# Kernel optimization log

Hardware: AMD Instinct MI355X
Metric: run time of the kernel (lower is better)

Reference implementation:

```python
import jax, jax.numpy as jnp
import numpy as np

EPS = 1e-6

def _rmsnorm(x, w):
    var = jnp.mean(x * x, axis=-1, keepdims=True)
    return w * (x * jax.lax.rsqrt(var + EPS))

def _rope(t, cos, sin):
    # t: [B,S,H,d_k]; cos/sin: [S,d_k/2] -> complex multiply on (even,odd) pairs
    B, S, H, D = t.shape
    tr = t.reshape(B, S, H, D // 2, 2)
    t0, t1 = tr[..., 0], tr[..., 1]
    c = cos[None, :, None, :]
    s = sin[None, :, None, :]
    o0 = t0 * c - t1 * s
    o1 = t0 * s + t1 * c
    return jnp.stack([o0, o1], axis=-1).reshape(B, S, H, D)

def setup_inputs() -> dict:
    key = jax.random.key(0)
    ks = jax.random.split(key, 9)
    B, S, D, H, DFF = 1, 4096, 1024, 16, 4096
    dk = D // H
    hidden = int(2 * DFF / 3)  # 2730, SwiGLU hidden dim
    sc = 0.02
    x = jax.random.normal(ks[0], (B, S, D), jnp.float32)
    # RoPE tables (theta=10000)
    inv_freq = 1.0 / (10000.0 ** (np.arange(0, dk, 2, dtype=np.float32) / dk))
    ang = np.outer(np.arange(S, dtype=np.float32), inv_freq)
    freqs_cos = jnp.asarray(np.cos(ang))
    freqs_sin = jnp.asarray(np.sin(ang))
    # causal additive mask [1,1,S,S]
    mask = jnp.where(np.tril(np.ones((S, S), bool)), 0.0, -1e9).astype(jnp.float32)[None, None]
    Wq = jax.random.normal(ks[1], (D, D), jnp.float32) * sc
    Wk = jax.random.normal(ks[2], (D, D), jnp.float32) * sc
    Wv = jax.random.normal(ks[3], (D, D), jnp.float32) * sc
    Wo = jax.random.normal(ks[4], (D, D), jnp.float32) * sc
    ln1_w = jnp.ones((D,), jnp.float32)
    ln2_w = jnp.ones((D,), jnp.float32)
    w1 = jax.random.normal(ks[5], (D, hidden), jnp.float32) * sc
    w2 = jax.random.normal(ks[6], (hidden, D), jnp.float32) * sc
    w3 = jax.random.normal(ks[7], (D, hidden), jnp.float32) * sc
    return dict(x=x, freqs_cos=freqs_cos, freqs_sin=freqs_sin, mask=mask,
                Wq=Wq, Wk=Wk, Wv=Wv, Wo=Wo, ln1_w=ln1_w, ln2_w=ln2_w,
                w1=w1, w2=w2, w3=w3)

def reference(x, freqs_cos, freqs_sin, mask, Wq, Wk, Wv, Wo, ln1_w, ln2_w, w1, w2, w3):
    B, S, D = x.shape
    H = 16
    dk = D // H
    scale = jnp.sqrt(jnp.float32(dk))
    # attention sublayer (pre-RMSNorm)
    h = _rmsnorm(x, ln1_w)
    Q = (h @ Wq).reshape(B, S, H, dk)
    K = (h @ Wk).reshape(B, S, H, dk)
    V = (h @ Wv).reshape(B, S, H, dk)
    Q = _rope(Q, freqs_cos, freqs_sin)
    K = _rope(K, freqs_cos, freqs_sin)
    scores = jnp.einsum('bshd,bthd->bhst', Q, K) / scale + mask  # [B,H,S,S]
    attn = jax.nn.softmax(scores, axis=-1)
    ctx = jnp.einsum('bhst,bthd->bshd', attn, V).reshape(B, S, D)
    x = x + ctx @ Wo
    # SwiGLU FFN sublayer
    h2 = _rmsnorm(x, ln2_w)
    ff = (jax.nn.silu(h2 @ w1) * (h2 @ w3)) @ w2
    x = x + ff
    return x
```

## Files before the change

### kernel.cpp

```cpp
#include <hip/hip_runtime.h>

#define S_LEN 4096
#define D_MODEL 1024
#define NHEAD 16
#define DK 64
#define HID 2730
#define HIDP 2880
#define QKV_LD 3072

typedef unsigned short u16;
typedef unsigned int u32;
typedef __bf16 bf16x8 __attribute__((ext_vector_type(8)));
typedef float f32x4 __attribute__((ext_vector_type(4)));

#define MFMA16 __builtin_amdgcn_mfma_f32_16x16x32_bf16
#define EXP2 __builtin_amdgcn_exp2f

__device__ __forceinline__ float b2f(u16 u) {
    return __builtin_bit_cast(float, (u32)u << 16);
}
__device__ __forceinline__ u16 f2b(float f) {
    u32 u = __builtin_bit_cast(u32, f);
    u += 0x7FFF + ((u >> 16) & 1);
    return (u16)(u >> 16);
}
__device__ __forceinline__ u32 pk_trunc(float lo, float hi) {
    return __builtin_amdgcn_perm(__builtin_bit_cast(u32, hi),
                                 __builtin_bit_cast(u32, lo), 0x07060302u);
}
__device__ __forceinline__ void gll16(const u16* g, u16* l) {
    __builtin_amdgcn_global_load_lds(
        (__attribute__((address_space(1))) void*)(g),
        (__attribute__((address_space(3))) void*)(l),
        16, 0, 0);
}

__global__ __launch_bounds__(256)
void prep_k(const float* s0, const float* s1, const float* s2,
            const float* s3, const float* s4, const float* s5,
            const float* s6, u16* d0, u16* d1, u16* d2, u16* d3,
            u16* d4, u16* d5, u16* d6,
            const float* __restrict__ x, const float* __restrict__ ln1,
            u16* __restrict__ hb) {
    __shared__ float t[32][33];
    __shared__ float red[4];
    const int bid = blockIdx.x;
    const int tid = threadIdx.x;

    if (bid >= 12736) {
        const int row = bid - 12736;
        const float4 v = ((const float4*)(x + (size_t)row * D_MODEL))[tid];
        float ss = v.x * v.x + v.y * v.y + v.z * v.z + v.w * v.w;
        for (int o = 32; o; o >>= 1) ss += __shfl_down(ss, o);
        if ((tid & 63) == 0) red[tid >> 6] = ss;
        __syncthreads();
        const float tot = red[0] + red[1] + red[2] + red[3];
        const float rs = rsqrtf(tot * (1.0f / D_MODEL) + 1e-6f);
        const float4 wv = ((const float4*)ln1)[tid];
        u16* op = hb + (size_t)row * D_MODEL + tid * 4;
        u32 p0 = (u32)f2b(v.x * rs * wv.x) | ((u32)f2b(v.y * rs * wv.y) << 16);
        u32 p1 = (u32)f2b(v.z * rs * wv.z) | ((u32)f2b(v.w * rs * wv.w) << 16);
        uint2 pk; pk.x = p0; pk.y = p1;
        *(uint2*)op = pk;
        return;
    }

    const float* srcs[7] = {s0, s1, s2, s3, s4, s5, s6};
    u16* dsts[7] = {d0, d1, d2, d3, d4, d5, d6};
    const int RR[7] = {1024, 1024, 1024, 1024, 1024, 1024, 2730};
    const int CC[7] = {1024, 1024, 1024, 1024, 2730, 2730, 1024};
    const int OC[7] = {1024, 1024, 1024, 1024, 1024, 1024, 2880};
    const int XD[7] = {32, 32, 32, 32, 32, 32, 90};

    int seg, start;
    if (bid < 4096)      { seg = bid >> 10; start = seg << 10; }
    else if (bid < 6976) { seg = 4; start = 4096; }
    else if (bid < 9856) { seg = 5; start = 6976; }
    else                 { seg = 6; start = 9856; }
    const int local = bid - start;
    const int bx = local % XD[seg], byy = local / XD[seg];
    const float* in = srcs[seg];
    u16* out = dsts[seg];
    const int R = RR[seg], C = CC[seg], outC = OC[seg];

    const int r0 = byy * 32;
    const int c0 = bx * 32;
    const int tx = tid & 31, ty = tid >> 5;
#pragma unroll
    for (int j = 0; j < 4; ++j) {
        int ir = c0 + ty + j * 8;
        int ic = r0 + tx;
        t[ty + j * 8][tx] = (ir < R && ic < C) ? in[(size_t)ir * C + ic] : 0.0f;
    }
    __syncthreads();
#pragma unroll
    for (int j = 0; j < 4; ++j)
        out[(size_t)(r0 + ty + j * 8) * outC + c0 + tx] = f2b(t[tx][ty + j * 8]);
}

__global__ __launch_bounds__(256)
void rmsnorm_k(const float* __restrict__ x, const float* __restrict__ w,
               u16* __restrict__ out) {
    const int row = blockIdx.x;
    const int tid = threadIdx.x;
    const float4 v = ((const float4*)(x + (size_t)row * D_MODEL))[tid];
    float ss = v.x * v.x + v.y * v.y + v.z * v.z + v.w * v.w;
    for (int o = 32; o; o >>= 1) ss += __shfl_down(ss, o);
    __shared__ float red[4];
    if ((tid & 63) == 0) red[tid >> 6] = ss;
    __syncthreads();
    const float tot = red[0] + red[1] + red[2] + red[3];
    const float rs = rsqrtf(tot * (1.0f / D_MODEL) + 1e-6f);
    const float4 wv = ((const float4*)w)[tid];
    u16* op = out + (size_t)row * D_MODEL + tid * 4;
    u32 p0 = (u32)f2b(v.x * rs * wv.x) | ((u32)f2b(v.y * rs * wv.y) << 16);
    u32 p1 = (u32)f2b(v.z * rs * wv.z) | ((u32)f2b(v.w * rs * wv.w) << 16);
    uint2 pk; pk.x = p0; pk.y = p1;
    *(uint2*)op = pk;
}

__global__ __launch_bounds__(256)
void packkv_k(const u16* __restrict__ qkv, const float* __restrict__ fc,
              const float* __restrict__ fs, u16* __restrict__ vt,
              u16* __restrict__ kp) {
    __shared__ u16 t[32][33];
    const int h = blockIdx.z;
    const int t0 = blockIdx.x * 32;
    const int d0 = blockIdx.y * 32;
    const int tx = threadIdx.x, ty = threadIdx.y;
#pragma unroll
    for (int j = 0; j < 4; ++j)
        t[ty + j * 8][tx] =
            qkv[(size_t)(t0 + ty + j * 8) * QKV_LD + 2 * D_MODEL + h * DK + d0 + tx];

    const int id = ty * 32 + tx;
    const int sA = t0 + (id >> 3);
    const int dA = d0 + (id & 7) * 4;
    uint2 kvp = *(const uint2*)(qkv + (size_t)sA * QKV_LD + D_MODEL + h * DK + dA);
    const int fi = sA * 32 + (dA >> 1);
    const float cc0 = fc[fi], ss0 = fs[fi];
    const float cc1 = fc[fi + 1], ss1 = fs[fi + 1];
    auto rpk = [](u32 w, float c, float s) -> u32 {
        const float a = b2f((u16)w), b = b2f((u16)(w >> 16));
        return (u32)f2b(a * c - b * s) | ((u32)f2b(a * s + b * c) << 16);
    };
    kvp.x = rpk(kvp.x, cc0, ss0);
    kvp.y = rpk(kvp.y, cc1, ss1);
    *(uint2*)(kp + ((size_t)h * S_LEN + sA) * DK + dA) = kvp;

    __syncthreads();
#pragma unroll
    for (int j = 0; j < 4; ++j)
        vt[(size_t)h * DK * S_LEN + (size_t)(d0 + ty + j * 8) * S_LEN + t0 + tx] =
            t[tx][ty + j * 8];
}

template <int EPI>
__global__ __launch_bounds__(256)
void gemm128(const u16* __restrict__ A, int lda, const u16* __restrict__ Bt, int ldb,
             void* __restrict__ C, int ldc, int K, const float* __restrict__ resid) {
    const int m0 = blockIdx.y * 128, n0 = blockIdx.x * 128;
    const int tid = threadIdx.x;
    const int wave = tid >> 6, lane = tid & 63;
    const int wr = wave >> 1, wc = wave & 1;
    const int r16 = lane & 15, kq = lane >> 4;

    __shared__ __align__(16) u16 As[128 * 32];
    __shared__ __align__(16) u16 Bs[128 * 32];

    const int srow = tid >> 2, sk = (tid & 3) * 8;
    const u16* ag0 = A + (size_t)(m0 + srow) * lda + sk;
    const u16* ag1 = A + (size_t)(m0 + 64 + srow) * lda + sk;
    const u16* bg0 = Bt + (size_t)(n0 + srow) * ldb + sk;
    const u16* bg1 = Bt + (size_t)(n0 + 64 + srow) * ldb + sk;
    u16* asw = As + wave * 512;
    u16* bsw = Bs + wave * 512;

    f32x4 acc[16];
#pragma unroll
    for (int i = 0; i < 16; ++i) acc[i] = f32x4{0.f, 0.f, 0.f, 0.f};

    for (int k0 = 0; k0 < K; k0 += 32) {
        __syncthreads();
        gll16(ag0 + k0, asw);
        gll16(ag1 + k0, asw + 2048);
        gll16(bg0 + k0, bsw);
        gll16(bg1 + k0, bsw + 2048);
        __syncthreads();
        bf16x8 af[4], bf[4];
#pragma unroll
        for (int mt = 0; mt < 4; ++mt)
            af[mt] = *(const bf16x8*)&As[(wr * 64 + mt * 16 + r16) * 32 + kq * 8];
#pragma unroll
        for (int nt = 0; nt < 4; ++nt)
            bf[nt] = *(const bf16x8*)&Bs[(wc * 64 + nt * 16 + r16) * 32 + kq * 8];
#pragma unroll
        for (int mt = 0; mt < 4; ++mt)
#pragma unroll
            for (int nt = 0; nt < 4; ++nt)
                acc[mt * 4 + nt] = MFMA16(af[mt], bf[nt], acc[mt * 4 + nt], 0, 0, 0);
    }

#pragma unroll
    for (int mt = 0; mt < 4; ++mt) {
#pragma unroll
        for (int nt = 0; nt < 4; ++nt) {
            const int col = n0 + wc * 64 + nt * 16 + r16;
#pragma unroll
            for (int j = 0; j < 4; ++j) {
                const int row = m0 + wr * 64 + mt * 16 + kq * 4 + j;
                if (EPI == 0) {
                    ((u16*)C)[(size_t)row * ldc + col] = f2b(acc[mt * 4 + nt][j]);
                } else {
                    ((float*)C)[(size_t)row * ldc + col] =
                        resid[(size_t)row * ldc + col] + acc[mt * 4 + nt][j];
                }
            }
        }
    }
}

__global__ __launch_bounds__(256)
void gemm64r(const u16* __restrict__ A, int lda, const u16* __restrict__ Bt, int ldb,
             float* __restrict__ C, int ldc, int K, const float* __restrict__ resid) {
    const int m0 = blockIdx.y * 128, n0 = blockIdx.x * 64;
    const int tid = threadIdx.x;
    const int wave = tid >> 6, lane = tid & 63;
    const int r16 = lane & 15, kq = lane >> 4;

    __shared__ __align__(16) u16 As[128 * 32];
    __shared__ __align__(16) u16 Bs[64 * 32];

    const int srow = tid >> 2, sk = (tid & 3) * 8;
    const u16* ag0 = A + (size_t)(m0 + srow) * lda + sk;
    const u16* ag1 = A + (size_t)(m0 + 64 + srow) * lda + sk;
    const u16* bg = Bt + (size_t)(n0 + srow) * ldb + sk;
    u16* asw = As + wave * 512;
    u16* bsw = Bs + wave * 512;

    f32x4 acc[8];
#pragma unroll
    for (int i = 0; i < 8; ++i) acc[i] = f32x4{0.f, 0.f, 0.f, 0.f};

    for (int k0 = 0; k0 < K; k0 += 32) {
        __syncthreads();
        gll16(ag0 + k0, asw);
        gll16(ag1 + k0, asw + 2048);
        gll16(bg + k0, bsw);
        __syncthreads();
        bf16x8 af[2], bf[4];
#pragma unroll
        for (int mt = 0; mt < 2; ++mt)
            af[mt] = *(const bf16x8*)&As[(wave * 32 + mt * 16 + r16) * 32 + kq * 8];
#pragma unroll
        for (int nt = 0; nt < 4; ++nt)
            bf[nt] = *(const bf16x8*)&Bs[(nt * 16 + r16) * 32 + kq * 8];
#pragma unroll
        for (int mt = 0; mt < 2; ++mt)
#pragma unroll
            for (int nt = 0; nt < 4; ++nt)
                acc[mt * 4 + nt] = MFMA16(af[mt], bf[nt], acc[mt * 4 + nt], 0, 0, 0);
    }

#pragma unroll
    for (int mt = 0; mt < 2; ++mt)
#pragma unroll
        for (int nt = 0; nt < 4; ++nt) {
            const int col = n0 + nt * 16 + r16;
#pragma unroll
            for (int j = 0; j < 4; ++j) {
                const int row = m0 + wave * 32 + mt * 16 + kq * 4 + j;
                C[(size_t)row * ldc + col] =
                    resid[(size_t)row * ldc + col] + acc[mt * 4 + nt][j];
            }
        }
}

__global__ __launch_bounds__(256, 3)
void gemm_dual96(const u16* __restrict__ A, int lda,
                 const u16* __restrict__ B1, const u16* __restrict__ B3, int ldb,
                 u16* __restrict__ C, int ldc, int K) {
    const int m0 = blockIdx.y * 128, n0 = blockIdx.x * 96;
    const int tid = threadIdx.x;
    const int wave = tid >> 6, lane = tid & 63;
    const int wr = wave >> 1, wc = wave & 1;
    const int r16 = lane & 15, kq = lane >> 4;

    __shared__ __align__(16) u16 As[128 * 32];
    __shared__ __align__(16) u16 Bs[192 * 32];

    const int srow = tid >> 2, sk = (tid & 3) * 8;
    const u16* ag0 = A + (size_t)(m0 + srow) * lda + sk;
    const u16* ag1 = A + (size_t)(m0 + 64 + srow) * lda + sk;
    const u16* bp0 = B1 + (size_t)(n0 + srow) * ldb + sk;
    const u16* bp1 = (srow < 32)
        ? B1 + (size_t)(n0 + 64 + srow) * ldb + sk
        : B3 + (size_t)(n0 + srow - 32) * ldb + sk;
    const u16* bp2 = B3 + (size_t)(n0 + 32 + srow) * ldb + sk;
    u16* asw0 = As + wave * 512;
    u16* asw1 = As + 2048 + wave * 512;
    u16* bsw0 = Bs + wave * 512;
    u16* bsw1 = Bs + 2048 + wave * 512;
    u16* bsw2 = Bs + 4096 + wave * 512;

    f32x4 acc1[12], acc3[12];
#pragma unroll
    for (int i = 0; i < 12; ++i) {
        acc1[i] = f32x4{0.f, 0.f, 0.f, 0.f};
        acc3[i] = f32x4{0.f, 0.f, 0.f, 0.f};
    }

    for (int k0 = 0; k0 < K; k0 += 32) {
        __syncthreads();
        gll16(ag0 + k0, asw0);
        gll16(ag1 + k0, asw1);
        gll16(bp0 + k0, bsw0);
        gll16(bp1 + k0, bsw1);
        gll16(bp2 + k0, bsw2);
        __syncthreads();
        bf16x8 af[4], b1f[3], b3f[3];
#pragma unroll
        for (int mt = 0; mt < 4; ++mt)
            af[mt] = *(const bf16x8*)&As[(wr * 64 + mt * 16 + r16) * 32 + kq * 8];
#pragma unroll
        for (int nt = 0; nt < 3; ++nt) {
            b1f[nt] = *(const bf16x8*)&Bs[(wc * 48 + nt * 16 + r16) * 32 + kq * 8];
            b3f[nt] = *(const bf16x8*)&Bs[(96 + wc * 48 + nt * 16 + r16) * 32 + kq * 8];
        }
#pragma unroll
        for (int mt = 0; mt < 4; ++mt)
#pragma unroll
            for (int nt = 0; nt < 3; ++nt) {
                acc1[mt * 3 + nt] = MFMA16(af[mt], b1f[nt], acc1[mt * 3 + nt], 0, 0, 0);
                acc3[mt * 3 + nt] = MFMA16(af[mt], b3f[nt], acc3[mt * 3 + nt], 0, 0, 0);
            }
    }

#pragma unroll
    for (int mt = 0; mt < 4; ++mt)
#pragma unroll
        for (int nt = 0; nt < 3; ++nt) {
            const int col = n0 + wc * 48 + nt * 16 + r16;
#pragma unroll
            for (int j = 0; j < 4; ++j) {
                const int row = m0 + wr * 64 + mt * 16 + kq * 4 + j;
                const float v1 = acc1[mt * 3 + nt][j];
                const float v3 = acc3[mt * 3 + nt][j];
                const float sig = 1.0f / (1.0f + __expf(-v1));
                C[(size_t)row * ldc + col] = f2b(v1 * sig * v3);
            }
        }
}

__global__ __launch_bounds__(256)
void flash_k(const u16* __restrict__ qkv, const u16* __restrict__ vt,
             const u16* __restrict__ kp, const float* __restrict__ fc,
             const float* __restrict__ fs, u16* __restrict__ ctx) {
    const int h = blockIdx.x;
    const int by = blockIdx.y;
    const int hi = by >> 4, lo = by & 15;
    const int base = lo + ((hi >> 1) << 4);
    const int qi = (hi & 1) ? (63 - base) : base;
    const int q0 = qi * 64;
    const int tid = threadIdx.x;
    const int wave = tid >> 6, lane = tid & 63;
    const int r16 = lane & 15, kq = lane >> 4;

    __shared__ __align__(16) u16 Kb[2][64 * 64];
    __shared__ __align__(16) u16 Vb[2][64 * 64];
    __shared__ __align__(16) u16 Ps[4 * 16 * 64];

    const u16* kb = kp + (size_t)h * S_LEN * DK;
    const u16* vb = vt + (size_t)h * DK * S_LEN;
    const int srow = tid >> 3;
    const int lcol = ((tid & 7) ^ (srow & 7)) * 8;
    const int qloc = wave * 16 + r16;
    const int qglob = q0 + qloc;
    const int sw = r16 & 7;
    const int c0 = (kq ^ sw) * 8;
    const int c1 = ((4 ^ kq) ^ sw) * 8;
    const int psw = r16 & 14;
    u16* psrow = Ps + wave * 1024 + r16 * 64;

    const float SC = 0.125f * 1.44269504f;
    const u16* qrow = qkv + (size_t)qglob * QKV_LD + h * DK;
    uint4 uq0 = *(const uint4*)(qrow + kq * 8);
    uint4 uq1 = *(const uint4*)(qrow + 32 + kq * 8);
    const float4 c0v = *(const float4*)(fc + qglob * 32 + kq * 4);
    const float4 s0v = *(const float4*)(fs + qglob * 32 + kq * 4);
    const float4 c1v = *(const float4*)(fc + qglob * 32 + 16 + kq * 4);
    const float4 s1v = *(const float4*)(fs + qglob * 32 + 16 + kq * 4);
    auto rp = [SC](u32 w, float c, float s) -> u32 {
        const float a = b2f((u16)w), b = b2f((u16)(w >> 16));
        return (u32)f2b((a * c - b * s) * SC) |
               ((u32)f2b((a * s + b * c) * SC) << 16);
    };
    uq0.x = rp(uq0.x, c0v.x, s0v.x); uq0.y = rp(uq0.y, c0v.y, s0v.y);
    uq0.z = rp(uq0.z, c0v.z, s0v.z); uq0.w = rp(uq0.w, c0v.w, s0v.w);
    uq1.x = rp(uq1.x, c1v.x, s1v.x); uq1.y = rp(uq1.y, c1v.y, s1v.y);
    uq1.z = rp(uq1.z, c1v.z, s1v.z); uq1.w = rp(uq1.w, c1v.w, s1v.w);
    const bf16x8 qf0 = __builtin_bit_cast(bf16x8, uq0);
    const bf16x8 qf1 = __builtin_bit_cast(bf16x8, uq1);

    f32x4 o[4];
#pragma unroll
    for (int i = 0; i < 4; ++i) o[i] = f32x4{0.f, 0.f, 0.f, 0.f};
    f32x4 lacc = f32x4{0.f, 0.f, 0.f, 0.f};
    const uint4 uone = make_uint4(0x3F803F80u, 0x3F803F80u, 0x3F803F80u, 0x3F803F80u);
    const bf16x8 ones = __builtin_bit_cast(bf16x8, uone);

#pragma unroll
    for (int i = 0; i < 2; ++i) {
        const int r = srow + i * 32;
        gll16(kb + (size_t)r * DK + lcol, Kb[0] + tid * 8 + i * 2048);
        gll16(vb + (size_t)r * S_LEN + lcol, Vb[0] + tid * 8 + i * 2048);
    }

    for (int t = 0; t <= qi; ++t) {
        __syncthreads();
        if (t < qi) {
            const int t1 = (t + 1) * 64;
            u16* kd = Kb[(t + 1) & 1];
            u16* vd = Vb[(t + 1) & 1];
#pragma unroll
            for (int i = 0; i < 2; ++i) {
                const int r = srow + i * 32;
                gll16(kb + (size_t)(t1 + r) * DK + lcol, kd + tid * 8 + i * 2048);
                gll16(vb + (size_t)r * S_LEN + t1 + lcol, vd + tid * 8 + i * 2048);
            }
        }
        const u16* Ks = Kb[t & 1];
        const u16* Vs = Vb[t & 1];

        f32x4 s[4];
#pragma unroll
        for (int nt = 0; nt < 4; ++nt) {
            s[nt] = f32x4{0.f, 0.f, 0.f, 0.f};
            const bf16x8 k0 = *(const bf16x8*)&Ks[(nt * 16 + r16) * 64 + c0];
            s[nt] = MFMA16(k0, qf0, s[nt], 0, 0, 0);
            const bf16x8 k1 = *(const bf16x8*)&Ks[(nt * 16 + r16) * 64 + c1];
            s[nt] = MFMA16(k1, qf1, s[nt], 0, 0, 0);
        }

        float pr[16];
#pragma unroll
        for (int nt = 0; nt < 4; ++nt)
#pragma unroll
            for (int j = 0; j < 4; ++j) pr[nt * 4 + j] = EXP2(s[nt][j]);
        if (t == qi) {
#pragma unroll
            for (int nt = 0; nt < 4; ++nt)
#pragma unroll
                for (int j = 0; j < 4; ++j)
                    if ((nt * 16 + kq * 4 + j) > qloc) pr[nt * 4 + j] = 0.f;
        }

#pragma unroll
        for (int nt = 0; nt < 4; ++nt) {
            uint2 pk;
            pk.x = pk_trunc(pr[nt * 4 + 0], pr[nt * 4 + 1]);
            pk.y = pk_trunc(pr[nt * 4 + 2], pr[nt * 4 + 3]);
            *(uint2*)&psrow[((nt * 4 + kq) ^ psw) * 4] = pk;
        }

#pragma unroll
        for (int ks = 0; ks < 2; ++ks) {
            const bf16x8 pf = *(const bf16x8*)&psrow[((8 * ks + 2 * kq) ^ psw) * 4];
            lacc = MFMA16(ones, pf, lacc, 0, 0, 0);
            const int cv = (((ks << 2) ^ kq) ^ sw) * 8;
#pragma unroll
            for (int nt = 0; nt < 4; ++nt) {
                const bf16x8 vf = *(const bf16x8*)&Vs[(nt * 16 + r16) * 64 + cv];
                o[nt] = MFMA16(vf, pf, o[nt], 0, 0, 0);
            }
        }
    }

    const float inv = 1.0f / lacc[0];
    const size_t row = qglob;
#pragma unroll
    for (int nt = 0; nt < 4; ++nt) {
        uint2 pk;
        pk.x = (u32)f2b(o[nt][0] * inv) | ((u32)f2b(o[nt][1] * inv) << 16);
        pk.y = (u32)f2b(o[nt][2] * inv) | ((u32)f2b(o[nt][3] * inv) << 16);
        *(uint2*)&ctx[row * D_MODEL + h * DK + nt * 16 + kq * 4] = pk;
    }
}

extern "C" void kernel_launch(void* const* d_in, const int* in_sizes, int n_in,
                              void* d_out, int out_size, void* d_ws, size_t ws_size,
                              hipStream_t stream) {
    const float* x    = (const float*)d_in[0];
    const float* fcos = (const float*)d_in[1];
    const float* fsin = (const float*)d_in[2];
    const float* Wq = (const float*)d_in[4];
    const float* Wk = (const float*)d_in[5];
    const float* Wv = (const float*)d_in[6];
    const float* Wo = (const float*)d_in[7];
    const float* ln1 = (const float*)d_in[8];
    const float* ln2 = (const float*)d_in[9];
    const float* w1 = (const float*)d_in[10];
    const float* w2 = (const float*)d_in[11];
    const float* w3 = (const float*)d_in[12];
    float* out = (float*)d_out;

    char* ws = (char*)d_ws;
    size_t off = 0;
    auto alloc = [&](size_t bytes) -> char* {
        char* p = ws + off;
        off += (bytes + 255) & ~(size_t)255;
        return p;
    };
    u16* hb    = (u16*)alloc((size_t)S_LEN * D_MODEL * 2);
    u16* wqkvt = (u16*)alloc((size_t)QKV_LD * D_MODEL * 2);
    u16* wot   = (u16*)alloc((size_t)D_MODEL * D_MODEL * 2);
    u16* qkvb  = (u16*)alloc((size_t)S_LEN * QKV_LD * 2);
    u16* vt    = (u16*)alloc((size_t)S_LEN * D_MODEL * 2);
    u16* kpack = (u16*)alloc((size_t)S_LEN * D_MODEL * 2);
    u16* ctxb  = (u16*)alloc((size_t)S_LEN * D_MODEL * 2);
    float* x2  = (float*)alloc((size_t)S_LEN * D_MODEL * 4);
    u16* h2b   = (u16*)alloc((size_t)S_LEN * D_MODEL * 2);
    u16* w1t   = (u16*)alloc((size_t)HIDP * D_MODEL * 2);
    u16* w3t   = (u16*)alloc((size_t)HIDP * D_MODEL * 2);
    u16* w2t   = (u16*)alloc((size_t)D_MODEL * HIDP * 2);
    u16* ffb   = (u16*)alloc((size_t)S_LEN * HIDP * 2);

    const dim3 tb32(32, 8);

    prep_k<<<16832, 256, 0, stream>>>(
        Wq, Wk, Wv, Wo, w1, w3, w2,
        wqkvt, wqkvt + (size_t)D_MODEL * D_MODEL,
        wqkvt + (size_t)2 * D_MODEL * D_MODEL, wot, w1t, w3t, w2t,
        x, ln1, hb);

    gemm128<0><<<dim3(QKV_LD / 128, S_LEN / 128), 256, 0, stream>>>(
        hb, D_MODEL, wqkvt, D_MODEL, qkvb, QKV_LD, D_MODEL, nullptr);

    packkv_k<<<dim3(S_LEN / 32, DK / 32, NHEAD), tb32, 0, stream>>>(
        qkvb, fcos, fsin, vt, kpack);

    flash_k<<<dim3(NHEAD, 64), 256, 0, stream>>>(qkvb, vt, kpack, fcos, fsin, ctxb);

    gemm64r<<<dim3(D_MODEL / 64, S_LEN / 128), 256, 0, stream>>>(
        ctxb, D_MODEL, wot, D_MODEL, x2, D_MODEL, D_MODEL, x);

    rmsnorm_k<<<S_LEN, 256, 0, stream>>>(x2, ln2, h2b);

    gemm_dual96<<<dim3(HIDP / 96, S_LEN / 128), 256, 0, stream>>>(
        h2b, D_MODEL, w1t, w3t, D_MODEL, ffb, HIDP, D_MODEL);

    gemm64r<<<dim3(D_MODEL / 64, S_LEN / 128), 256, 0, stream>>>(
        ffb, HIDP, w2t, HIDP, out, D_MODEL, HIDP, x2);
}
```

Measured before the change: 416.4 us.

## Pair causal query tiles per flash block and deepen dual GEMM K-tile

New measurement: 427.3 us. 1.03x slower.

```diff
diff --git a/kernel.cpp b/kernel.cpp
--- a/kernel.cpp
+++ b/kernel.cpp
@@ -277,31 +277,32 @@
 }
 
 __global__ __launch_bounds__(256, 3)
-void gemm_dual96(const u16* __restrict__ A, int lda,
-                 const u16* __restrict__ B1, const u16* __restrict__ B3, int ldb,
-                 u16* __restrict__ C, int ldc, int K) {
+void gemm_dual96x(const u16* __restrict__ A, int lda,
+                  const u16* __restrict__ B1, const u16* __restrict__ B3, int ldb,
+                  u16* __restrict__ C, int ldc, int K) {
     const int m0 = blockIdx.y * 128, n0 = blockIdx.x * 96;
     const int tid = threadIdx.x;
     const int wave = tid >> 6, lane = tid & 63;
     const int wr = wave >> 1, wc = wave & 1;
     const int r16 = lane & 15, kq = lane >> 4;
 
-    __shared__ __align__(16) u16 As[128 * 32];
-    __shared__ __align__(16) u16 Bs[192 * 32];
-
-    const int srow = tid >> 2, sk = (tid & 3) * 8;
-    const u16* ag0 = A + (size_t)(m0 + srow) * lda + sk;
-    const u16* ag1 = A + (size_t)(m0 + 64 + srow) * lda + sk;
-    const u16* bp0 = B1 + (size_t)(n0 + srow) * ldb + sk;
-    const u16* bp1 = (srow < 32)
-        ? B1 + (size_t)(n0 + 64 + srow) * ldb + sk
-        : B3 + (size_t)(n0 + srow - 32) * ldb + sk;
-    const u16* bp2 = B3 + (size_t)(n0 + 32 + srow) * ldb + sk;
-    u16* asw0 = As + wave * 512;
-    u16* asw1 = As + 2048 + wave * 512;
-    u16* bsw0 = Bs + wave * 512;
-    u16* bsw1 = Bs + 2048 + wave * 512;
-    u16* bsw2 = Bs + 4096 + wave * 512;
+    __shared__ __align__(16) u16 As[128 * 64];
+    __shared__ __align__(16) u16 Bs[192 * 64];
+
+    const int srow = tid >> 3;
+    const int scol = ((tid & 7) ^ (srow & 7)) * 8;
+    const u16* ag0 = A + (size_t)(m0 +  0 + srow) * lda + scol;
+    const u16* ag1 = A + (size_t)(m0 + 32 + srow) * lda + scol;
+    const u16* ag2 = A + (size_t)(m0 + 64 + srow) * lda + scol;
+    const u16* ag3 = A + (size_t)(m0 + 96 + srow) * lda + scol;
+    const u16* bg0 = B1 + (size_t)(n0 +  0 + srow) * ldb + scol;
+    const u16* bg1 = B1 + (size_t)(n0 + 32 + srow) * ldb + scol;
+    const u16* bg2 = B1 + (size_t)(n0 + 64 + srow) * ldb + scol;
+    const u16* bg3 = B3 + (size_t)(n0 +  0 + srow) * ldb + scol;
+    const u16* bg4 = B3 + (size_t)(n0 + 32 + srow) * ldb + scol;
+    const u16* bg5 = B3 + (size_t)(n0 + 64 + srow) * ldb + scol;
+    u16* const ad = As + tid * 8;
+    u16* const bd = Bs + tid * 8;
 
     f32x4 acc1[12], acc3[12];
 #pragma unroll
@@ -310,30 +311,40 @@
         acc3[i] = f32x4{0.f, 0.f, 0.f, 0.f};
     }
 
-    for (int k0 = 0; k0 < K; k0 += 32) {
-        __syncthreads();
-        gll16(ag0 + k0, asw0);
-        gll16(ag1 + k0, asw1);
-        gll16(bp0 + k0, bsw0);
-        gll16(bp1 + k0, bsw1);
-        gll16(bp2 + k0, bsw2);
-        __syncthreads();
-        bf16x8 af[4], b1f[3], b3f[3];
-#pragma unroll
-        for (int mt = 0; mt < 4; ++mt)
-            af[mt] = *(const bf16x8*)&As[(wr * 64 + mt * 16 + r16) * 32 + kq * 8];
-#pragma unroll
-        for (int nt = 0; nt < 3; ++nt) {
-            b1f[nt] = *(const bf16x8*)&Bs[(wc * 48 + nt * 16 + r16) * 32 + kq * 8];
-            b3f[nt] = *(const bf16x8*)&Bs[(96 + wc * 48 + nt * 16 + r16) * 32 + kq * 8];
-        }
-#pragma unroll
-        for (int mt = 0; mt < 4; ++mt)
+    const int rsw = r16 & 7;
+    for (int k0 = 0; k0 < K; k0 += 64) {
+        __syncthreads();
+        gll16(ag0 + k0, ad);
+        gll16(ag1 + k0, ad + 2048);
+        gll16(ag2 + k0, ad + 4096);
+        gll16(ag3 + k0, ad + 6144);
+        gll16(bg0 + k0, bd);
+        gll16(bg1 + k0, bd + 2048);
+        gll16(bg2 + k0, bd + 4096);
+        gll16(bg3 + k0, bd + 6144);
+        gll16(bg4 + k0, bd + 8192);
+        gll16(bg5 + k0, bd + 10240);
+        __syncthreads();
+#pragma unroll
+        for (int ks = 0; ks < 2; ++ks) {
+            const int slot = (((ks << 2) | kq) ^ rsw) * 8;
+            bf16x8 af[4], b1f[3], b3f[3];
+#pragma unroll
+            for (int mt = 0; mt < 4; ++mt)
+                af[mt] = *(const bf16x8*)&As[(wr * 64 + mt * 16 + r16) * 64 + slot];
 #pragma unroll
             for (int nt = 0; nt < 3; ++nt) {
-                acc1[mt * 3 + nt] = MFMA16(af[mt], b1f[nt], acc1[mt * 3 + nt], 0, 0, 0);
-                acc3[mt * 3 + nt] = MFMA16(af[mt], b3f[nt], acc3[mt * 3 + nt], 0, 0, 0);
+                b1f[nt] = *(const bf16x8*)&Bs[(wc * 48 + nt * 16 + r16) * 64 + slot];
+                b3f[nt] = *(const bf16x8*)&Bs[(96 + wc * 48 + nt * 16 + r16) * 64 + slot];
             }
+#pragma unroll
+            for (int mt = 0; mt < 4; ++mt)
+#pragma unroll
+                for (int nt = 0; nt < 3; ++nt) {
+                    acc1[mt * 3 + nt] = MFMA16(af[mt], b1f[nt], acc1[mt * 3 + nt], 0, 0, 0);
+                    acc3[mt * 3 + nt] = MFMA16(af[mt], b3f[nt], acc3[mt * 3 + nt], 0, 0, 0);
+                }
+        }
     }
 
 #pragma unroll
@@ -357,11 +368,8 @@
              const u16* __restrict__ kp, const float* __restrict__ fc,
              const float* __restrict__ fs, u16* __restrict__ ctx) {
     const int h = blockIdx.x;
-    const int by = blockIdx.y;
-    const int hi = by >> 4, lo = by & 15;
-    const int base = lo + ((hi >> 1) << 4);
-    const int qi = (hi & 1) ? (63 - base) : base;
-    const int q0 = qi * 64;
+    const int pair = blockIdx.y;
+    const int qa = pair, qb = 63 - pair;
     const int tid = threadIdx.x;
     const int wave = tid >> 6, lane = tid & 63;
     const int r16 = lane & 15, kq = lane >> 4;
@@ -375,7 +383,6 @@
     const int srow = tid >> 3;
     const int lcol = ((tid & 7) ^ (srow & 7)) * 8;
     const int qloc = wave * 16 + r16;
-    const int qglob = q0 + qloc;
     const int sw = r16 & 7;
     const int c0 = (kq ^ sw) * 8;
     const int c1 = ((4 ^ kq) ^ sw) * 8;
@@ -383,31 +390,85 @@
     u16* psrow = Ps + wave * 1024 + r16 * 64;
 
     const float SC = 0.125f * 1.44269504f;
-    const u16* qrow = qkv + (size_t)qglob * QKV_LD + h * DK;
-    uint4 uq0 = *(const uint4*)(qrow + kq * 8);
-    uint4 uq1 = *(const uint4*)(qrow + 32 + kq * 8);
-    const float4 c0v = *(const float4*)(fc + qglob * 32 + kq * 4);
-    const float4 s0v = *(const float4*)(fs + qglob * 32 + kq * 4);
-    const float4 c1v = *(const float4*)(fc + qglob * 32 + 16 + kq * 4);
-    const float4 s1v = *(const float4*)(fs + qglob * 32 + 16 + kq * 4);
     auto rp = [SC](u32 w, float c, float s) -> u32 {
         const float a = b2f((u16)w), b = b2f((u16)(w >> 16));
         return (u32)f2b((a * c - b * s) * SC) |
                ((u32)f2b((a * s + b * c) * SC) << 16);
     };
-    uq0.x = rp(uq0.x, c0v.x, s0v.x); uq0.y = rp(uq0.y, c0v.y, s0v.y);
-    uq0.z = rp(uq0.z, c0v.z, s0v.z); uq0.w = rp(uq0.w, c0v.w, s0v.w);
-    uq1.x = rp(uq1.x, c1v.x, s1v.x); uq1.y = rp(uq1.y, c1v.y, s1v.y);
-    uq1.z = rp(uq1.z, c1v.z, s1v.z); uq1.w = rp(uq1.w, c1v.w, s1v.w);
-    const bf16x8 qf0 = __builtin_bit_cast(bf16x8, uq0);
-    const bf16x8 qf1 = __builtin_bit_cast(bf16x8, uq1);
-
-    f32x4 o[4];
-#pragma unroll
-    for (int i = 0; i < 4; ++i) o[i] = f32x4{0.f, 0.f, 0.f, 0.f};
-    f32x4 lacc = f32x4{0.f, 0.f, 0.f, 0.f};
+    auto loadq = [&](int qglob, bf16x8& q0out, bf16x8& q1out) {
+        const u16* qrow = qkv + (size_t)qglob * QKV_LD + h * DK;
+        uint4 uq0 = *(const uint4*)(qrow + kq * 8);
+        uint4 uq1 = *(const uint4*)(qrow + 32 + kq * 8);
+        const float4 c0v = *(const float4*)(fc + qglob * 32 + kq * 4);
+        const float4 s0v = *(const float4*)(fs + qglob * 32 + kq * 4);
+        const float4 c1v = *(const float4*)(fc + qglob * 32 + 16 + kq * 4);
+        const float4 s1v = *(const float4*)(fs + qglob * 32 + 16 + kq * 4);
+        uq0.x = rp(uq0.x, c0v.x, s0v.x); uq0.y = rp(uq0.y, c0v.y, s0v.y);
+        uq0.z = rp(uq0.z, c0v.z, s0v.z); uq0.w = rp(uq0.w, c0v.w, s0v.w);
+        uq1.x = rp(uq1.x, c1v.x, s1v.x); uq1.y = rp(uq1.y, c1v.y, s1v.y);
+        uq1.z = rp(uq1.z, c1v.z, s1v.z); uq1.w = rp(uq1.w, c1v.w, s1v.w);
+        q0out = __builtin_bit_cast(bf16x8, uq0);
+        q1out = __builtin_bit_cast(bf16x8, uq1);
+    };
+    const int qgA = qa * 64 + qloc;
+    const int qgB = qb * 64 + qloc;
+    bf16x8 qfA0, qfA1, qfB0, qfB1;
+    loadq(qgA, qfA0, qfA1);
+    loadq(qgB, qfB0, qfB1);
+
+    f32x4 oA[4], oB[4];
+#pragma unroll
+    for (int i = 0; i < 4; ++i) {
+        oA[i] = f32x4{0.f, 0.f, 0.f, 0.f};
+        oB[i] = f32x4{0.f, 0.f, 0.f, 0.f};
+    }
+    f32x4 laccA = f32x4{0.f, 0.f, 0.f, 0.f};
+    f32x4 laccB = f32x4{0.f, 0.f, 0.f, 0.f};
     const uint4 uone = make_uint4(0x3F803F80u, 0x3F803F80u, 0x3F803F80u, 0x3F803F80u);
     const bf16x8 ones = __builtin_bit_cast(bf16x8, uone);
+
+    auto tilec = [&](const u16* Ks, const u16* Vs, const bf16x8& q0f,
+                     const bf16x8& q1f, f32x4 (&o)[4], f32x4& lacc, bool dmask) {
+        f32x4 s[4];
+#pragma unroll
+        for (int nt = 0; nt < 4; ++nt) {
+            s[nt] = f32x4{0.f, 0.f, 0.f, 0.f};
+            const bf16x8 k0 = *(const bf16x8*)&Ks[(nt * 16 + r16) * 64 + c0];
+            s[nt] = MFMA16(k0, q0f, s[nt], 0, 0, 0);
+            const bf16x8 k1 = *(const bf16x8*)&Ks[(nt * 16 + r16) * 64 + c1];
+            s[nt] = MFMA16(k1, q1f, s[nt], 0, 0, 0);
+        }
+        float pr[16];
+#pragma unroll
+        for (int nt = 0; nt < 4; ++nt)
+#pragma unroll
+            for (int j = 0; j < 4; ++j) pr[nt * 4 + j] = EXP2(s[nt][j]);
+        if (dmask) {
+#pragma unroll
+            for (int nt = 0; nt < 4; ++nt)
+#pragma unroll
+                for (int j = 0; j < 4; ++j)
+                    if ((nt * 16 + kq * 4 + j) > qloc) pr[nt * 4 + j] = 0.f;
+        }
+#pragma unroll
+        for (int nt = 0; nt < 4; ++nt) {
+            uint2 pk;
+            pk.x = pk_trunc(pr[nt * 4 + 0], pr[nt * 4 + 1]);
+            pk.y = pk_trunc(pr[nt * 4 + 2], pr[nt * 4 + 3]);
+            *(uint2*)&psrow[((nt * 4 + kq) ^ psw) * 4] = pk;
+        }
+#pragma unroll
+        for (int ks = 0; ks < 2; ++ks) {
+            const bf16x8 pf = *(const bf16x8*)&psrow[((8 * ks + 2 * kq) ^ psw) * 4];
+            lacc = MFMA16(ones, pf, lacc, 0, 0, 0);
+            const int cv = (((ks << 2) ^ kq) ^ sw) * 8;
+#pragma unroll
+            for (int nt = 0; nt < 4; ++nt) {
+                const bf16x8 vf = *(const bf16x8*)&Vs[(nt * 16 + r16) * 64 + cv];
+                o[nt] = MFMA16(vf, pf, o[nt], 0, 0, 0);
+            }
+        }
+    };
 
 #pragma unroll
     for (int i = 0; i < 2; ++i) {
@@ -416,9 +477,9 @@
         gll16(vb + (size_t)r * S_LEN + lcol, Vb[0] + tid * 8 + i * 2048);
     }
 
-    for (int t = 0; t <= qi; ++t) {
-        __syncthreads();
-        if (t < qi) {
+    for (int t = 0; t <= qb; ++t) {
+        __syncthreads();
+        if (t < qb) {
             const int t1 = (t + 1) * 64;
             u16* kd = Kb[(t + 1) & 1];
             u16* vd = Vb[(t + 1) & 1];
@@ -432,59 +493,24 @@
         const u16* Ks = Kb[t & 1];
         const u16* Vs = Vb[t & 1];
 
-        f32x4 s[4];
-#pragma unroll
-        for (int nt = 0; nt < 4; ++nt) {
-            s[nt] = f32x4{0.f, 0.f, 0.f, 0.f};
-            const bf16x8 k0 = *(const bf16x8*)&Ks[(nt * 16 + r16) * 64 + c0];
-            s[nt] = MFMA16(k0, qf0, s[nt], 0, 0, 0);
-            const bf16x8 k1 = *(const bf16x8*)&Ks[(nt * 16 + r16) * 64 + c1];
-            s[nt] = MFMA16(k1, qf1, s[nt], 0, 0, 0);
-        }
-
-        float pr[16];
-#pragma unroll
-        for (int nt = 0; nt < 4; ++nt)
-#pragma unroll
-            for (int j = 0; j < 4; ++j) pr[nt * 4 + j] = EXP2(s[nt][j]);
-        if (t == qi) {
-#pragma unroll
-            for (int nt = 0; nt < 4; ++nt)
-#pragma unroll
-                for (int j = 0; j < 4; ++j)
-                    if ((nt * 16 + kq * 4 + j) > qloc) pr[nt * 4 + j] = 0.f;
-        }
-
+        tilec(Ks, Vs, qfB0, qfB1, oB, laccB, t == qb);
+        if (t <= qa)
+            tilec(Ks, Vs, qfA0, qfA1, oA, laccA, t == qa);
+    }
+
+    auto wout = [&](f32x4 (&o)[4], float lsum, int qg) {
+        const float inv = 1.0f / lsum;
+        const size_t row = qg;
 #pragma unroll
         for (int nt = 0; nt < 4; ++nt) {
             uint2 pk;
-            pk.x = pk_trunc(pr[nt * 4 + 0], pr[nt * 4 + 1]);
-            pk.y = pk_trunc(pr[nt * 4 + 2], pr[nt * 4 + 3]);
-            *(uint2*)&psrow[((nt * 4 + kq) ^ psw) * 4] = pk;
-        }
-
-#pragma unroll
-        for (int ks = 0; ks < 2; ++ks) {
-            const bf16x8 pf = *(const bf16x8*)&psrow[((8 * ks + 2 * kq) ^ psw) * 4];
-            lacc = MFMA16(ones, pf, lacc, 0, 0, 0);
-            const int cv = (((ks << 2) ^ kq) ^ sw) * 8;
-#pragma unroll
-            for (int nt = 0; nt < 4; ++nt) {
-                const bf16x8 vf = *(const bf16x8*)&Vs[(nt * 16 + r16) * 64 + cv];
-                o[nt] = MFMA16(vf, pf, o[nt], 0, 0, 0);
-            }
-        }
-    }
-
-    const float inv = 1.0f / lacc[0];
-    const size_t row = qglob;
-#pragma unroll
-    for (int nt = 0; nt < 4; ++nt) {
-        uint2 pk;
-        pk.x = (u32)f2b(o[nt][0] * inv) | ((u32)f2b(o[nt][1] * inv) << 16);
-        pk.y = (u32)f2b(o[nt][2] * inv) | ((u32)f2b(o[nt][3] * inv) << 16);
-        *(uint2*)&ctx[row * D_MODEL + h * DK + nt * 16 + kq * 4] = pk;
-    }
+            pk.x = (u32)f2b(o[nt][0] * inv) | ((u32)f2b(o[nt][1] * inv) << 16);
+            pk.y = (u32)f2b(o[nt][2] * inv) | ((u32)f2b(o[nt][3] * inv) << 16);
+            *(uint2*)&ctx[row * D_MODEL + h * DK + nt * 16 + kq * 4] = pk;
+        }
+    };
+    wout(oA, laccA[0], qgA);
+    wout(oB, laccB[0], qgB);
 }
 
 extern "C" void kernel_launch(void* const* d_in, const int* in_sizes, int n_in,
@@ -539,14 +565,14 @@
     packkv_k<<<dim3(S_LEN / 32, DK / 32, NHEAD), tb32, 0, stream>>>(
         qkvb, fcos, fsin, vt, kpack);
 
-    flash_k<<<dim3(NHEAD, 64), 256, 0, stream>>>(qkvb, vt, kpack, fcos, fsin, ctxb);
+    flash_k<<<dim3(NHEAD, 32), 256, 0, stream>>>(qkvb, vt, kpack, fcos, fsin, ctxb);
 
     gemm64r<<<dim3(D_MODEL / 64, S_LEN / 128), 256, 0, stream>>>(
         ctxb, D_MODEL, wot, D_MODEL, x2, D_MODEL, D_MODEL, x);
 
     rmsnorm_k<<<S_LEN, 256, 0, stream>>>(x2, ln2, h2b);
 
-    gemm_dual96<<<dim3(HIDP / 96, S_LEN / 128), 256, 0, stream>>>(
+    gemm_dual96x<<<dim3(HIDP / 96, S_LEN / 128), 256, 0, stream>>>(
         h2b, D_MODEL, w1t, w3t, D_MODEL, ffb, HIDP, D_MODEL);
 
     gemm64r<<<dim3(D_MODEL / 64, S_LEN / 128), 256, 0, stream>>>(
```
